# Optimization experiments

Hardware: AMD Instinct MI355X
Metric: run time of the kernel (lower is better)

The kernel has to match this reference:

```python
import jax, jax.numpy as jnp
import numpy as np

B, N, K = 8, 2048, 20
NC = 50
EPS = 1e-5
SLOPE = 0.2


def _knn(xt, k):
    # xt: [B, N, C]; negative squared euclidean distance, top-k (includes self)
    xx = jnp.sum(xt * xt, axis=-1)                      # [B, N]
    inner = jnp.einsum('bnc,bmc->bnm', xt, xt)          # [B, N, N]
    dist = 2.0 * inner - xx[:, :, None] - xx[:, None, :]
    return jax.lax.top_k(dist, k)[1]                    # [B, N, k] int32


def _edge_conv(xt, w, g, b, k):
    # xt: [B, N, C]; w: [O, 2C]; BatchNorm2d over (B, N, k) per out-channel.
    idx = _knn(xt, k)
    nbr = xt[jnp.arange(B)[:, None, None], idx]          # [B, N, k, C]
    ctr = jnp.broadcast_to(xt[:, :, None, :], nbr.shape)
    edge = jnp.concatenate([nbr - ctr, ctr], axis=-1)    # [B, N, k, 2C]
    h = jnp.einsum('bnkc,oc->bnko', edge, w)             # 1x1 conv, no bias
    mu = jnp.mean(h, axis=(0, 1, 2))
    var = jnp.var(h, axis=(0, 1, 2))
    h = (h - mu) / jnp.sqrt(var + EPS) * g + b
    h = jnp.where(h > 0, h, SLOPE * h)                   # LeakyReLU(0.2)
    return jnp.max(h, axis=2)                            # max over k -> [B, N, O]


def _bn1d(y, g, b):
    mu = jnp.mean(y, axis=0)
    var = jnp.var(y, axis=0)
    return (y - mu) / jnp.sqrt(var + EPS) * g + b


def setup_inputs() -> dict:
    key = jax.random.key(0)
    ks = jax.random.split(key, 20)

    def rn(k, shape, scale):
        return jax.random.normal(k, shape, dtype=jnp.float32) * scale

    d = {
        'x': rn(ks[0], (B * N, 3), 1.0),
        'pos': rn(ks[1], (B * N, 3), 1.0),
        'batch': jnp.repeat(jnp.arange(B, dtype=jnp.int64), N),
        'edge_index': jax.random.randint(ks[2], (2, B * N), 0, B * N, dtype=jnp.int64),
        # EdgeConv 1x1 conv weights [out, in], BN gamma/beta
        'w1': rn(ks[3], (64, 6), 0.3),   'g1': jnp.ones(64),  'b1': jnp.zeros(64),
        'w2': rn(ks[4], (64, 128), 0.1), 'g2': jnp.ones(64),  'b2': jnp.zeros(64),
        'w3': rn(ks[5], (128, 128), 0.1),'g3': jnp.ones(128), 'b3': jnp.zeros(128),
        'w4': rn(ks[6], (256, 256), 0.08),'g4': jnp.ones(256),'b4': jnp.zeros(256),
        # lin1: Linear(512,1024)+ReLU+BN1d(1024)
        'lw1': rn(ks[7], (512, 1024), 0.04), 'lb1': jnp.zeros(1024),
        'lg1': jnp.ones(1024), 'lbb1': jnp.zeros(1024),
        # mlp: [1024->256 +ReLU+BN] -> [256->128 +ReLU+BN] -> Lin(128, NC)
        'mw1': rn(ks[8], (1024, 256), 0.03), 'mb1': jnp.zeros(256),
        'mg1': jnp.ones(256), 'mbb1': jnp.zeros(256),
        'mw2': rn(ks[9], (256, 128), 0.06), 'mb2': jnp.zeros(128),
        'mg2': jnp.ones(128), 'mbb2': jnp.zeros(128),
        'hw': rn(ks[10], (128, NC), 0.09), 'hb': jnp.zeros(NC),
    }
    return d


def reference(x, pos, batch, edge_index,
              w1, g1, b1, w2, g2, b2, w3, g3, b3, w4, g4, b4,
              lw1, lb1, lg1, lbb1,
              mw1, mb1, mg1, mbb1, mw2, mb2, mg2, mbb2,
              hw, hb):
    # batch is sorted with N points per cloud -> static reshape
    xt = x.reshape(B, N, 3)
    x1 = _edge_conv(xt, w1, g1, b1, K)   # [B, N, 64]
    x2 = _edge_conv(x1, w2, g2, b2, K)   # [B, N, 64]
    x3 = _edge_conv(x2, w3, g3, b3, K)   # [B, N, 128]
    x4 = _edge_conv(x3, w4, g4, b4, K)   # [B, N, 256]
    cat = jnp.concatenate([x1, x2, x3, x4], axis=-1)  # [B, N, 512]
    h = cat.reshape(B * N, 512)
    h = _bn1d(jax.nn.relu(h @ lw1 + lb1), lg1, lbb1)
    h = _bn1d(jax.nn.relu(h @ mw1 + mb1), mg1, mbb1)   # dropout = identity (eval)
    h = _bn1d(jax.nn.relu(h @ mw2 + mb2), mg2, mbb2)
    logits = h @ hw + hb
    return jax.nn.log_softmax(logits, axis=1)
```

## Files before the change

### kernel.cpp

```cpp
#include <hip/hip_runtime.h>
#include <math.h>

#define NB 8
#define NP 2048
#define KNBR 20
#define NROWS (NB*NP)
#define SLOPEV 0.2f
#define EPSV 1e-5f

typedef short s8v __attribute__((ext_vector_type(8)));
typedef float f4v __attribute__((ext_vector_type(4)));
typedef double d4v __attribute__((ext_vector_type(4)));

__device__ __forceinline__ unsigned short f2bf(float f) {
    union { float f; unsigned u; } v; v.f = f;
    unsigned r = v.u + 0x7FFFu + ((v.u >> 16) & 1u);
    return (unsigned short)(r >> 16);
}

__global__ void mfma64_probe(int* __restrict__ tab)
{
    const int lane = threadIdx.x;
    d4v z = {0.0, 0.0, 0.0, 0.0};
    d4v pa = __builtin_amdgcn_mfma_f64_16x16x4f64((double)lane, 1.0, z, 0, 0, 0);
    d4v pb = __builtin_amdgcn_mfma_f64_16x16x4f64(1.0, (double)lane, z, 0, 0, 0);
    int famA = 1, famB = 1;
#pragma unroll
    for (int r = 0; r < 4; ++r) {
        int iv = (int)(pa[r] + 0.5);
        int row;
        if ((iv & 3) == 0 && iv >= 96) row = (iv - 96) >> 2;
        else { row = (iv - 6) >> 4; famA = 0; }
        int jv = (int)(pb[r] + 0.5);
        int col;
        if ((jv & 3) == 0 && jv >= 96) col = (jv - 96) >> 2;
        else { col = (jv - 6) >> 4; famB = 0; }
        tab[lane * 8 + r]     = row;
        tab[lane * 8 + 4 + r] = col;
    }
    tab[512 + lane] = famA;
    tab[576 + lane] = famB;
}

template<int KD>
__global__ __launch_bounds__(256, 2) void knn_fused2(
    const double* __restrict__ F, int lda, int C,
    const double* __restrict__ xx,
    double* __restrict__ tmpv, int* __restrict__ tmpc,
    const int* __restrict__ tab)
{
    constexpr int CH = (KD < 16) ? KD : 32;
    __shared__ double Bs[CH][66];
    __shared__ double Tile[64][65];
    __shared__ double thr[64];
    __shared__ unsigned msk[64][2];

    const int tid = threadIdx.x;
    const int wave = tid >> 6, lane = tid & 63;
    const int bb    = blockIdx.z;
    const int half  = blockIdx.y;
    const int r0    = blockIdx.x * 64;
    const int cbase = half * 1024;
    const double* Fb  = F  + (size_t)bb * NP * lda;
    const double* xxb = xx + (size_t)bb * NP;

    int rT[4], cT[4];
#pragma unroll
    for (int r = 0; r < 4; ++r) { rT[r] = tab[lane * 8 + r]; cT[r] = tab[lane * 8 + 4 + r]; }
    const int famA = tab[512];
    const int famB = tab[576];
    const int am = famA ? (lane & 15) : (lane >> 2);
    const int ak = famA ? (lane >> 4) : (lane & 3);
    const int bn = famB ? (lane & 15) : (lane >> 2);
    const int bk = famB ? (lane >> 4) : (lane & 3);

    const int arow = r0 + wave * 16 + am;
    double areg[KD / 4];
#pragma unroll
    for (int j = 0; j < KD / 4; ++j) {
        const int k = j * 4 + ak;
        areg[j] = (k < C) ? Fb[(size_t)arow * lda + k] : 0.0;
    }
    double xr4[4];
#pragma unroll
    for (int rg = 0; rg < 4; ++rg)
        xr4[rg] = xxb[r0 + wave * 16 + rT[rg]];

    double kv[KNBR];
    int    ki[KNBR];
#pragma unroll
    for (int q = 0; q < KNBR; ++q) { kv[q] = -INFINITY; ki[q] = 0; }
    if (tid < 64) { thr[tid] = -INFINITY; msk[tid][0] = 0u; msk[tid][1] = 0u; }
    __syncthreads();

    for (int ct = 0; ct < 16; ++ct) {
        const int c0 = cbase + ct * 64;
        d4v acc[4];
#pragma unroll
        for (int nt = 0; nt < 4; ++nt) acc[nt] = (d4v){0.0, 0.0, 0.0, 0.0};

#pragma unroll
        for (int kc = 0; kc < KD; kc += CH) {
            {
                const int col = tid >> 2;
                const int kb0 = (tid & 3) * (CH / 4);
                const double* bp = Fb + (size_t)(c0 + col) * lda + kc + kb0;
#pragma unroll
                for (int i = 0; i < CH / 4; ++i) {
                    const int k2 = kc + kb0 + i;
                    Bs[kb0 + i][col] = (k2 < C) ? bp[i] : 0.0;
                }
            }
            __syncthreads();
#pragma unroll
            for (int kg = 0; kg < CH / 4; ++kg) {
                const double a  = areg[kc / 4 + kg];
                const double b0 = Bs[kg * 4 + bk][bn];
                const double b1 = Bs[kg * 4 + bk][16 + bn];
                const double b2 = Bs[kg * 4 + bk][32 + bn];
                const double b3 = Bs[kg * 4 + bk][48 + bn];
                acc[0] = __builtin_amdgcn_mfma_f64_16x16x4f64(a, b0, acc[0], 0, 0, 0);
                acc[1] = __builtin_amdgcn_mfma_f64_16x16x4f64(a, b1, acc[1], 0, 0, 0);
                acc[2] = __builtin_amdgcn_mfma_f64_16x16x4f64(a, b2, acc[2], 0, 0, 0);
                acc[3] = __builtin_amdgcn_mfma_f64_16x16x4f64(a, b3, acc[3], 0, 0, 0);
            }
            __syncthreads();
        }

#pragma unroll
        for (int nt = 0; nt < 4; ++nt) {
#pragma unroll
            for (int rg = 0; rg < 4; ++rg) {
                const int rloc = wave * 16 + rT[rg];
                const int cloc = nt * 16 + cT[rg];
                const double d = (2.0 * acc[nt][rg] - xr4[rg]) - xxb[c0 + cloc];
                if (d > thr[rloc]) {
                    Tile[rloc][cloc] = d;
                    atomicOr(&msk[rloc][cloc >> 5], 1u << (cloc & 31));
                }
            }
        }
        __syncthreads();

        if (tid < 64) {
            bool changed = false;
#pragma unroll
            for (int w2 = 0; w2 < 2; ++w2) {
                unsigned m = msk[tid][w2];
                msk[tid][w2] = 0u;
                while (m) {
                    const int b = __ffs(m) - 1;
                    m &= m - 1u;
                    const double v = Tile[tid][w2 * 32 + b];
                    if (v > kv[KNBR - 1]) {
                        const int col = c0 + w2 * 32 + b;
                        int pos = 0;
#pragma unroll
                        for (int q = 0; q < KNBR; ++q) pos += (kv[q] >= v) ? 1 : 0;
#pragma unroll
                        for (int q = KNBR - 1; q >= 0; --q) {
                            if (q > pos)       { kv[q] = kv[q - 1]; ki[q] = ki[q - 1]; }
                            else if (q == pos) { kv[q] = v;         ki[q] = col; }
                        }
                        changed = true;
                    }
                }
            }
            if (changed) thr[tid] = kv[KNBR - 1];
        }
        __syncthreads();
    }

    if (tid < 64) {
        const size_t rowg = (size_t)bb * NP + r0 + tid;
        double* vp = tmpv + (rowg * 2 + half) * KNBR;
        int*    cp = tmpc + (rowg * 2 + half) * KNBR;
#pragma unroll
        for (int q = 0; q < KNBR; ++q) { vp[q] = kv[q]; cp[q] = ki[q]; }
    }
}

__global__ void merge_topk(const double* __restrict__ tmpv,
                           const int* __restrict__ tmpc,
                           int* __restrict__ out)
{
    const int row = blockIdx.x * 256 + threadIdx.x;
    if (row >= NROWS) return;
    const double* va = tmpv + (size_t)row * 2 * KNBR;
    const int*    ca = tmpc + (size_t)row * 2 * KNBR;
    const double* vb = va + KNBR;
    const int*    cb = ca + KNBR;
    const int jbase = (row / NP) * NP;
    int* op = out + (size_t)row * KNBR;
    int ia = 0, ib = 0;
#pragma unroll
    for (int q = 0; q < KNBR; ++q) {
        const double x = va[ia], y = vb[ib];
        const bool takeA = (x > y) || (x == y && ca[ia] < cb[ib]);
        if (takeA) { op[q] = jbase + ca[ia]; ++ia; }
        else       { op[q] = jbase + cb[ib]; ++ib; }
    }
}

#define DK 16
__global__ __launch_bounds__(256, 2) void gemm64(
    const double* __restrict__ A, int lda,
    const double* __restrict__ Bm, int ldb,
    double* __restrict__ P, double* __restrict__ Q, int O, int Kd,
    const int* __restrict__ tab)
{
    __shared__ double As[DK][130];
    __shared__ double Bs[DK][66];
    const int tid = threadIdx.x;
    const int wave = tid >> 6, lane = tid & 63;
    const int quad = lane >> 4, l15 = lane & 15;
    const int row0 = blockIdx.y * 128, col0 = blockIdx.x * 64;

    int rT[4], cT[4];
#pragma unroll
    for (int r = 0; r < 4; ++r) { rT[r] = tab[lane * 8 + r]; cT[r] = tab[lane * 8 + 4 + r]; }
    const int famA = tab[512];
    const int famB = tab[576];
    const int am = famA ? l15 : (lane >> 2);
    const int ak = famA ? quad : (lane & 3);
    const int bn = famB ? l15 : (lane >> 2);
    const int bk = famB ? quad : (lane & 3);

    d4v acc[2][4];
#pragma unroll
    for (int mt = 0; mt < 2; ++mt)
#pragma unroll
        for (int nt = 0; nt < 4; ++nt) acc[mt][nt] = (d4v){0.0, 0.0, 0.0, 0.0};

    const int ma = tid >> 1, ka = (tid & 1) * 8;
    const int mb = tid >> 2, kb = (tid & 3) * 4;

    for (int kc = 0; kc < Kd; kc += DK) {
        const double* ap = A + (size_t)(row0 + ma) * lda + kc + ka;
#pragma unroll
        for (int i = 0; i < 8; ++i) {
            const int k2 = kc + ka + i;
            As[ka + i][ma] = (k2 < Kd) ? ap[i] : 0.0;
        }
        const double* bp = Bm + (size_t)(col0 + mb) * ldb + kc + kb;
#pragma unroll
        for (int i = 0; i < 4; ++i) {
            const int k2 = kc + kb + i;
            Bs[kb + i][mb] = (k2 < Kd) ? bp[i] : 0.0;
        }
        __syncthreads();
#pragma unroll
        for (int kg = 0; kg < 4; ++kg) {
            const int k = kg * 4;
            double a0 = As[k + ak][wave * 32 + am];
            double a1 = As[k + ak][wave * 32 + 16 + am];
            double b0 = Bs[k + bk][bn];
            double b1 = Bs[k + bk][16 + bn];
            double b2 = Bs[k + bk][32 + bn];
            double b3 = Bs[k + bk][48 + bn];
            acc[0][0] = __builtin_amdgcn_mfma_f64_16x16x4f64(a0, b0, acc[0][0], 0, 0, 0);
            acc[0][1] = __builtin_amdgcn_mfma_f64_16x16x4f64(a0, b1, acc[0][1], 0, 0, 0);
            acc[0][2] = __builtin_amdgcn_mfma_f64_16x16x4f64(a0, b2, acc[0][2], 0, 0, 0);
            acc[0][3] = __builtin_amdgcn_mfma_f64_16x16x4f64(a0, b3, acc[0][3], 0, 0, 0);
            acc[1][0] = __builtin_amdgcn_mfma_f64_16x16x4f64(a1, b0, acc[1][0], 0, 0, 0);
            acc[1][1] = __builtin_amdgcn_mfma_f64_16x16x4f64(a1, b1, acc[1][1], 0, 0, 0);
            acc[1][2] = __builtin_amdgcn_mfma_f64_16x16x4f64(a1, b2, acc[1][2], 0, 0, 0);
            acc[1][3] = __builtin_amdgcn_mfma_f64_16x16x4f64(a1, b3, acc[1][3], 0, 0, 0);
        }
        __syncthreads();
    }

    double* dst = (col0 < O) ? P : Q;
    const int cbase = (col0 < O) ? col0 : (col0 - O);
#pragma unroll
    for (int mt = 0; mt < 2; ++mt)
#pragma unroll
        for (int nt = 0; nt < 4; ++nt) {
#pragma unroll
            for (int rg = 0; rg < 4; ++rg) {
                const int r = row0 + wave * 32 + mt * 16 + rT[rg];
                const int c = cbase + nt * 16 + cT[rg];
                dst[(size_t)r * O + c] = acc[mt][nt][rg];
            }
        }
}

__global__ __launch_bounds__(256) void gemm_bf16(
    const float* __restrict__ A, int lda,
    const unsigned short* __restrict__ W,
    float* __restrict__ C, int ldc,
    int Kd,
    const float* __restrict__ bias,
    const float* __restrict__ a_ss)
{
    __shared__ unsigned short As[4][64][8];
    __shared__ unsigned short Bs[4][128][8];
    const int tid = threadIdx.x;
    const int wave = tid >> 6, lane = tid & 63;
    const int quad = lane >> 4, l15 = lane & 15;
    const int row0 = blockIdx.y * 64, col0 = blockIdx.x * 128;

    f4v acc[4][2];
#pragma unroll
    for (int mt = 0; mt < 4; ++mt)
#pragma unroll
        for (int nt = 0; nt < 2; ++nt) acc[mt][nt] = (f4v){0.f, 0.f, 0.f, 0.f};

    const int ar = tid >> 2, akc = tid & 3;
    const int br = tid >> 1, bkc = (tid & 1) * 2;

    for (int kc0 = 0; kc0 < Kd; kc0 += 32) {
        {
            const float* ap = A + (size_t)(row0 + ar) * lda + kc0 + akc * 8;
            float t0[8];
            *(float4*)&t0[0] = *(const float4*)ap;
            *(float4*)&t0[4] = *(const float4*)(ap + 4);
            if (a_ss) {
                const int kb = kc0 + akc * 8;
#pragma unroll
                for (int i = 0; i < 8; ++i)
                    t0[i] = fmaf(t0[i], a_ss[kb + i], a_ss[Kd + kb + i]);
            }
            unsigned short u[8];
#pragma unroll
            for (int i = 0; i < 8; ++i) u[i] = f2bf(t0[i]);
            *(uint4*)&As[akc][ar][0] = *(const uint4*)&u[0];
        }
        {
            const unsigned short* wp = W + (size_t)(col0 + br) * Kd + kc0 + bkc * 8;
            uint4 q0 = *(const uint4*)wp;
            uint4 q1 = *(const uint4*)(wp + 8);
            *(uint4*)&Bs[bkc][br][0]     = q0;
            *(uint4*)&Bs[bkc + 1][br][0] = q1;
        }
        __syncthreads();

        s8v a[4], b[2];
#pragma unroll
        for (int mt = 0; mt < 4; ++mt)
            a[mt] = *(const s8v*)&As[quad][mt * 16 + l15][0];
#pragma unroll
        for (int nt = 0; nt < 2; ++nt)
            b[nt] = *(const s8v*)&Bs[quad][wave * 32 + nt * 16 + l15][0];
#pragma unroll
        for (int mt = 0; mt < 4; ++mt)
#pragma unroll
            for (int nt = 0; nt < 2; ++nt)
                acc[mt][nt] = __builtin_amdgcn_mfma_f32_16x16x32_bf16(
                    a[mt], b[nt], acc[mt][nt], 0, 0, 0);
        __syncthreads();
    }

#pragma unroll
    for (int mt = 0; mt < 4; ++mt)
#pragma unroll
        for (int nt = 0; nt < 2; ++nt) {
            const int col = col0 + wave * 32 + nt * 16 + l15;
            const float bi = bias[col];
#pragma unroll
            for (int r = 0; r < 4; ++r) {
                const int row = row0 + mt * 16 + quad * 4 + r;
                float v = acc[mt][nt][r] + bi;
                v = fmaxf(v, 0.f);
                C[(size_t)row * ldc + col] = v;
            }
        }
}

#define GBK 16
__global__ __launch_bounds__(256, 2) void gemm_f32(
    const float* __restrict__ A, int lda,
    const float* __restrict__ Bm, int ldb,
    float* __restrict__ Cm, int ldc,
    int M, int Nn, int Kd, int mode,
    const float* __restrict__ bias,
    const float* __restrict__ a_ss)
{
    __shared__ float As[GBK][132];
    __shared__ float Bs[GBK][132];
    const int tid = threadIdx.x;
    const int tx = tid & 15, ty = tid >> 4;
    const int lin = blockIdx.y * gridDim.x + blockIdx.x;
    const int bx = lin / gridDim.y;
    const int by = lin - bx * gridDim.y;
    const int row0 = by * 128, col0 = bx * 128;
    float acc[8][8];
#pragma unroll
    for (int i = 0; i < 8; ++i)
#pragma unroll
        for (int j = 0; j < 8; ++j) acc[i][j] = 0.f;

    const int m  = tid >> 1;
    const int kk = (tid & 1) * 8;

    for (int kc = 0; kc < Kd; kc += GBK) {
        const int gc = col0 + m;
        const float* ap = A  + (size_t)(row0 + m) * lda + kc + kk;
        const float* bp = Bm + (size_t)gc * ldb + kc + kk;
#pragma unroll
        for (int i = 0; i < 8; ++i) {
            const int k2 = kc + kk + i;
            float v = 0.f;
            if (k2 < Kd) {
                v = ap[i];
                if (a_ss) v = fmaf(v, a_ss[k2], a_ss[Kd + k2]);
            }
            As[kk + i][m] = v;
        }
#pragma unroll
        for (int i = 0; i < 8; ++i) {
            const int k2 = kc + kk + i;
            float v = 0.f;
            if (gc < Nn && k2 < Kd) v = bp[i];
            Bs[kk + i][m] = v;
        }
        __syncthreads();
#pragma unroll
        for (int k = 0; k < GBK; ++k) {
            float4 a0 = *(const float4*)&As[k][ty * 4];
            float4 a1 = *(const float4*)&As[k][64 + ty * 4];
            float4 b0 = *(const float4*)&Bs[k][tx * 4];
            float4 b1 = *(const float4*)&Bs[k][64 + tx * 4];
            float a[8] = {a0.x, a0.y, a0.z, a0.w, a1.x, a1.y, a1.z, a1.w};
            float b[8] = {b0.x, b0.y, b0.z, b0.w, b1.x, b1.y, b1.z, b1.w};
#pragma unroll
            for (int i = 0; i < 8; ++i)
#pragma unroll
                for (int j = 0; j < 8; ++j) acc[i][j] = fmaf(a[i], b[j], acc[i][j]);
        }
        __syncthreads();
    }

#pragma unroll
    for (int i = 0; i < 8; ++i) {
        const int row = row0 + ty * 4 + (i & 3) + ((i >> 2) << 6);
        if (row >= M) continue;
#pragma unroll
        for (int h = 0; h < 2; ++h) {
            const int c0 = col0 + tx * 4 + (h << 6);
#pragma unroll
            for (int j = 0; j < 4; ++j) {
                const int col = c0 + j;
                if (col < Nn) {
                    float t = acc[i][h * 4 + j];
                    if (mode == 2)      t = fmaxf(t + bias[col], 0.f);
                    else if (mode == 3) t = t + bias[col];
                    Cm[(size_t)row * ldc + col] = t;
                }
            }
        }
    }
}

__global__ void f2d_kernel(const float* __restrict__ in, double* __restrict__ out, long n)
{
    long t = (long)blockIdx.x * 256 + threadIdx.x;
    if (t < n) out[t] = (double)in[t];
}
__global__ void d2f_kernel(const double* __restrict__ in, float* __restrict__ out, long n)
{
    long t = (long)blockIdx.x * 256 + threadIdx.x;
    if (t < n) out[t] = (float)in[t];
}

__global__ void xx_kernel_d(const double* __restrict__ F, int lda, int C,
                            double* __restrict__ xx)
{
    int r = blockIdx.x * 256 + threadIdx.x;
    if (r >= NROWS) return;
    const double* p = F + (long)r * lda;
    double s = 0.0;
    for (int c = 0; c < C; ++c) { double v = p[c]; s = fma(v, v, s); }
    xx[r] = s;
}

__global__ void wmod_kernel_d(const float* __restrict__ w, double* __restrict__ wm,
                              int O, int C)
{
    int t = blockIdx.x * 256 + threadIdx.x;
    if (t >= O * C) return;
    int o = t / C, c = t - o * C;
    double a = (double)w[o * 2 * C + c];
    double b = (double)w[o * 2 * C + C + c];
    wm[o * C + c] = a;
    wm[(O + o) * C + c] = b - a;
}

__global__ void transpose_kernel(const float* __restrict__ in, float* __restrict__ out,
                                 int R, int C)
{
    long t = (long)blockIdx.x * 256 + threadIdx.x;
    if (t >= (long)R * C) return;
    int r = (int)(t / C), c = (int)(t - (long)r * C);
    out[(long)c * R + r] = in[t];
}

__global__ void transpose_bf(const float* __restrict__ in, unsigned short* __restrict__ out,
                             int R, int C)
{
    long t = (long)blockIdx.x * 256 + threadIdx.x;
    if (t >= (long)R * C) return;
    int r = (int)(t / C), c = (int)(t - (long)r * C);
    out[(long)c * R + r] = f2bf(in[t]);
}

__global__ __launch_bounds__(256) void edge_gather(const double* __restrict__ P,
                                                   const double* __restrict__ Q,
                                                   const int* __restrict__ idx,
                                                   int O, int shiftO,
                                                   double* __restrict__ sums,
                                                   double* __restrict__ catOut, int ldo)
{
    const int tid = threadIdx.x;
    const int o = tid & (O - 1);
    const int q = tid >> shiftO;
    const int nsub = 256 >> shiftO;
    const int lin = blockIdx.x;
    const int r0 = (lin & 7) * NP + (lin >> 3) * 16;
    double s = 0.0, ss = 0.0;
    for (int r = r0 + q; r < r0 + 16; r += nsub) {
        const double qv = Q[(size_t)r * O + o];
        const int* ip = idx + r * KNBR;
        double m = -INFINITY;
        for (int k = 0; k < KNBR; ++k) {
            const int j = ip[k];
            const double v = P[(size_t)j * O + o] + qv;
            s += v; ss = fma(v, v, ss);
            m = fmax(m, v);
        }
        catOut[(size_t)r * ldo + o] = m;
    }
    __shared__ double red[256];
    red[tid] = s; __syncthreads();
    if (q == 0) for (int qq = 1; qq < nsub; ++qq) s += red[o + (qq << shiftO)];
    __syncthreads();
    red[tid] = ss; __syncthreads();
    if (q == 0) {
        for (int qq = 1; qq < nsub; ++qq) ss += red[o + (qq << shiftO)];
        atomicAdd(&sums[o], s);
        atomicAdd(&sums[O + o], ss);
    }
}

__global__ void bn_finalize_d(const double* __restrict__ sums,
                              const float* __restrict__ g, const float* __restrict__ b,
                              double* __restrict__ ss, int O, double invCnt)
{
    int o = blockIdx.x * 256 + threadIdx.x;
    if (o >= O) return;
    double mu  = sums[o] * invCnt;
    double var = sums[O + o] * invCnt - mu * mu;
    double is  = 1.0 / sqrt(var + 1e-5);
    double sc  = (double)g[o] * is;
    ss[o] = sc;
    ss[O + o] = (double)b[o] - mu * sc;
}

__global__ __launch_bounds__(256) void bn_apply(double* __restrict__ catOut, int ldo,
                                                const double* __restrict__ ssb,
                                                int O, int shiftO,
                                                const double* __restrict__ P,
                                                const double* __restrict__ Q,
                                                const int* __restrict__ idx)
{
    const int t = blockIdx.x * 256 + threadIdx.x;
    const int o = t & (O - 1);
    const int r = t >> shiftO;
    const double sc = ssb[o], sh = ssb[O + o];
    double v = catOut[(size_t)r * ldo + o];
    if (sc < 0.0) {
        const double qv = Q[(size_t)r * O + o];
        const int* ip = idx + r * KNBR;
        double m = INFINITY;
        for (int k = 0; k < KNBR; ++k)
            m = fmin(m, P[(size_t)ip[k] * O + o] + qv);
        v = m;
    }
    double u = fma(v, sc, sh);
    u = u > 0.0 ? u : 0.2 * u;
    catOut[(size_t)r * ldo + o] = u;
}

__global__ void col_stats(const float* __restrict__ Y, int ncol,
                          float* __restrict__ sums)
{
    int c  = blockIdx.x * 128 + threadIdx.x;
    int r0 = blockIdx.y * 256;
    float s = 0.f, ss = 0.f;
    for (int r = r0; r < r0 + 256; ++r) {
        float v = Y[(long)r * ncol + c];
        s += v; ss = fmaf(v, v, ss);
    }
    atomicAdd(&sums[c], s);
    atomicAdd(&sums[ncol + c], ss);
}

__global__ void bn_finalize_f(const float* __restrict__ sums,
                              const float* __restrict__ g, const float* __restrict__ b,
                              float* __restrict__ ss, int O, float invCnt)
{
    int o = blockIdx.x * 256 + threadIdx.x;
    if (o >= O) return;
    float mu  = sums[o] * invCnt;
    float var = sums[O + o] * invCnt - mu * mu;
    float is  = rsqrtf(var + EPSV);
    float sc  = g[o] * is;
    ss[o] = sc;
    ss[O + o] = b[o] - mu * sc;
}

__global__ __launch_bounds__(256) void log_softmax_kernel(float* __restrict__ Y)
{
    const int lane = threadIdx.x & 63;
    const int row  = blockIdx.x * 4 + (threadIdx.x >> 6);
    float v = -INFINITY;
    if (lane < 50) v = Y[(long)row * 50 + lane];
    float mx = v;
#pragma unroll
    for (int off = 32; off >= 1; off >>= 1) mx = fmaxf(mx, __shfl_xor(mx, off, 64));
    float e = (lane < 50) ? expf(v - mx) : 0.f;
    float s = e;
#pragma unroll
    for (int off = 32; off >= 1; off >>= 1) s += __shfl_xor(s, off, 64);
    float l = logf(s) + mx;
    if (lane < 50) Y[(long)row * 50 + lane] = v - l;
}

extern "C" void kernel_launch(void* const* d_in, const int* in_sizes, int n_in,
                              void* d_out, int out_size, void* d_ws, size_t ws_size,
                              hipStream_t stream)
{
    const float* x   = (const float*)d_in[0];
    const float* w[4]  = {(const float*)d_in[4], (const float*)d_in[7],
                          (const float*)d_in[10], (const float*)d_in[13]};
    const float* g[4]  = {(const float*)d_in[5], (const float*)d_in[8],
                          (const float*)d_in[11], (const float*)d_in[14]};
    const float* bb[4] = {(const float*)d_in[6], (const float*)d_in[9],
                          (const float*)d_in[12], (const float*)d_in[15]};
    const float* lw1 = (const float*)d_in[16]; const float* lb1 = (const float*)d_in[17];
    const float* lg1 = (const float*)d_in[18]; const float* lbb1 = (const float*)d_in[19];
    const float* mw1 = (const float*)d_in[20]; const float* mb1 = (const float*)d_in[21];
    const float* mg1 = (const float*)d_in[22]; const float* mbb1 = (const float*)d_in[23];
    const float* mw2 = (const float*)d_in[24]; const float* mb2 = (const float*)d_in[25];
    const float* mg2 = (const float*)d_in[26]; const float* mbb2 = (const float*)d_in[27];
    const float* hw  = (const float*)d_in[28]; const float* hb  = (const float*)d_in[29];
    float* out = (float*)d_out;

    char* base = (char*)d_ws;
    double* catD = (double*)base;
    char*  un    = base + 67108864;
    double* tmpv = (double*)un;
    int*    tmpc = (int*)(un + 5242880);
    double* Pb   = (double*)un;
    double* Qb   = (double*)(un + 33554432);
    float* cat32 = (float*)un;
    float* Y2    = (float*)(un + 33554432);
    float* Y3    = (float*)(un + 50331648);
    unsigned short* lw1Tb = (unsigned short*)(un + 58720256);
    unsigned short* mw1Tb = (unsigned short*)(un + 59768832);
    unsigned short* mw2Tb = (unsigned short*)(un + 60293120);
    float* hwT   = (float*)(un + 60358656);
    float* Y1    = (float*)base;
    char* tail = base + 2u * 67108864u;
    int*    idxb  = (int*)tail;
    double* xD    = (double*)(tail + 1310720);
    double* xxD   = (double*)(tail + 1703936);
    double* wmodD = (double*)(tail + 1835008);
    double* sumsD = (double*)(tail + 2359296);
    double* ssbD  = (double*)(tail + 2367488);
    float*  sumsF = (float*)(tail + 2375680);
    float*  ssbF  = (float*)(tail + 2383872);
    int*    mtab  = (int*)(tail + 2392064);

    mfma64_probe<<<1, 64, 0, stream>>>(mtab);

    f2d_kernel<<<(NROWS * 3 + 255) / 256, 256, 0, stream>>>(x, xD, (long)NROWS * 3);

    const double* Fin[4] = {xD, catD + 0, catD + 64, catD + 128};
    const int   ldaL[4] = {3, 512, 512, 512};
    const int   CL[4]   = {3, 64, 64, 128};
    const int   OL[4]   = {64, 64, 128, 256};
    const int   coff[4] = {0, 64, 128, 256};

    for (int l = 0; l < 4; ++l) {
        const double* F = Fin[l];
        const int lda = ldaL[l], C = CL[l], O = OL[l];
        const int shiftO = (O == 64) ? 6 : (O == 128) ? 7 : 8;

        wmod_kernel_d<<<(O * C + 255) / 256, 256, 0, stream>>>(w[l], wmodD, O, C);
        xx_kernel_d<<<NROWS / 256, 256, 0, stream>>>(F, lda, C, xxD);

        dim3 kg(NP / 64, 2, NB);
        if (C == 3)
            knn_fused2<4><<<kg, 256, 0, stream>>>(F, lda, C, xxD, tmpv, tmpc, mtab);
        else if (C == 64)
            knn_fused2<64><<<kg, 256, 0, stream>>>(F, lda, C, xxD, tmpv, tmpc, mtab);
        else
            knn_fused2<128><<<kg, 256, 0, stream>>>(F, lda, C, xxD, tmpv, tmpc, mtab);
        merge_topk<<<NROWS / 256, 256, 0, stream>>>(tmpv, tmpc, idxb);

        gemm64<<<dim3((2 * O) / 64, NROWS / 128), 256, 0, stream>>>(
            F, lda, wmodD, C, Pb, Qb, O, C, mtab);

        hipMemsetAsync(sumsD, 0, 2 * O * sizeof(double), stream);
        edge_gather<<<NROWS / 16, 256, 0, stream>>>(Pb, Qb, idxb, O, shiftO, sumsD,
                                                    catD + coff[l], 512);
        bn_finalize_d<<<(O + 255) / 256, 256, 0, stream>>>(sumsD, g[l], bb[l], ssbD, O,
                                                           1.0 / ((double)NROWS * KNBR));
        bn_apply<<<(NROWS * O) / 256, 256, 0, stream>>>(catD + coff[l], 512, ssbD,
                                                        O, shiftO, Pb, Qb, idxb);
    }

    d2f_kernel<<<((long)NROWS * 512 + 255) / 256, 256, 0, stream>>>(catD, cat32, (long)NROWS * 512);

    transpose_bf<<<(512 * 1024 + 255) / 256, 256, 0, stream>>>(lw1, lw1Tb, 512, 1024);
    transpose_bf<<<(1024 * 256 + 255) / 256, 256, 0, stream>>>(mw1, mw1Tb, 1024, 256);
    transpose_bf<<<(256 * 128 + 255) / 256, 256, 0, stream>>>(mw2, mw2Tb, 256, 128);
    transpose_kernel<<<(128 * 50 + 255) / 256, 256, 0, stream>>>(hw, hwT, 128, 50);

    {
        gemm_bf16<<<dim3(1024 / 128, NROWS / 64), 256, 0, stream>>>(
            cat32, 512, lw1Tb, Y1, 1024, 512, lb1, nullptr);
        hipMemsetAsync(sumsF, 0, 2 * 1024 * sizeof(float), stream);
        col_stats<<<dim3(1024 / 128, 64), 128, 0, stream>>>(Y1, 1024, sumsF);
        bn_finalize_f<<<4, 256, 0, stream>>>(sumsF, lg1, lbb1, ssbF, 1024, 1.f / NROWS);
    }
    {
        gemm_bf16<<<dim3(256 / 128, NROWS / 64), 256, 0, stream>>>(
            Y1, 1024, mw1Tb, Y2, 256, 1024, mb1, ssbF);
        hipMemsetAsync(sumsF, 0, 2 * 256 * sizeof(float), stream);
        col_stats<<<dim3(256 / 128, 64), 128, 0, stream>>>(Y2, 256, sumsF);
        bn_finalize_f<<<1, 256, 0, stream>>>(sumsF, mg1, mbb1, ssbF, 256, 1.f / NROWS);
    }
    {
        gemm_bf16<<<dim3(128 / 128, NROWS / 64), 256, 0, stream>>>(
            Y2, 256, mw2Tb, Y3, 128, 256, mb2, ssbF);
        hipMemsetAsync(sumsF, 0, 2 * 128 * sizeof(float), stream);
        col_stats<<<dim3(1, 64), 128, 0, stream>>>(Y3, 128, sumsF);
        bn_finalize_f<<<1, 256, 0, stream>>>(sumsF, mg2, mbb2, ssbF, 128, 1.f / NROWS);
    }
    {
        dim3 gg(1, NROWS / 128);
        gemm_f32<<<gg, 256, 0, stream>>>(Y3, 128, hwT, 128, out, 50,
                                         NROWS, 50, 128, 3, hb, ssbF);
        log_softmax_kernel<<<NROWS / 4, 256, 0, stream>>>(out);
    }
}
```

Baseline: 1.922 ms.

## Double-buffer B tile loads in fused kNN MFMA kernel

Replaces the single shared-memory B chunk buffer with two buffers. The next chunk, or the first chunk of the next column tile, is prefetched while MFMA runs on the current one, which removes one barrier per chunk. The chunk depth is reduced from 32 to 16 so the double buffer fits in shared memory, which means more iterations and barriers for the deep layers. The aim is to hide global-load latency behind the f64 matrix work.

```diff
diff --git a/kernel.cpp b/kernel.cpp
--- a/kernel.cpp
+++ b/kernel.cpp
@@ -49,8 +49,9 @@
     double* __restrict__ tmpv, int* __restrict__ tmpc,
     const int* __restrict__ tab)
 {
-    constexpr int CH = (KD < 16) ? KD : 32;
-    __shared__ double Bs[CH][66];
+    constexpr int CH  = (KD < 16) ? KD : 16;
+    constexpr int NCH = KD / CH;
+    __shared__ double Bs[2][CH][66];
     __shared__ double Tile[64][65];
     __shared__ double thr[64];
     __shared__ unsigned msk[64][2];
@@ -74,6 +75,9 @@
     const int bn = famB ? (lane & 15) : (lane >> 2);
     const int bk = famB ? (lane >> 4) : (lane & 3);
 
+    const int scol = tid >> 2;
+    const int skb0 = (tid & 3) * (CH / 4);
+
     const int arow = r0 + wave * 16 + am;
     double areg[KD / 4];
 #pragma unroll
@@ -91,8 +95,18 @@
 #pragma unroll
     for (int q = 0; q < KNBR; ++q) { kv[q] = -INFINITY; ki[q] = 0; }
     if (tid < 64) { thr[tid] = -INFINITY; msk[tid][0] = 0u; msk[tid][1] = 0u; }
+
+    {
+        const double* bp = Fb + (size_t)(cbase + scol) * lda + skb0;
+#pragma unroll
+        for (int i = 0; i < CH / 4; ++i) {
+            const int k2 = skb0 + i;
+            Bs[0][skb0 + i][scol] = (k2 < C) ? bp[i] : 0.0;
+        }
+    }
     __syncthreads();
 
+    int cur = 0;
     for (int ct = 0; ct < 16; ++ct) {
         const int c0 = cbase + ct * 64;
         d4v acc[4];
@@ -100,31 +114,37 @@
         for (int nt = 0; nt < 4; ++nt) acc[nt] = (d4v){0.0, 0.0, 0.0, 0.0};
 
 #pragma unroll
-        for (int kc = 0; kc < KD; kc += CH) {
-            {
-                const int col = tid >> 2;
-                const int kb0 = (tid & 3) * (CH / 4);
-                const double* bp = Fb + (size_t)(c0 + col) * lda + kc + kb0;
+        for (int ich = 0; ich < NCH; ++ich) {
+            if (ich + 1 < NCH) {
+                const int kc2 = (ich + 1) * CH;
+                const double* bp = Fb + (size_t)(c0 + scol) * lda + kc2 + skb0;
 #pragma unroll
                 for (int i = 0; i < CH / 4; ++i) {
-                    const int k2 = kc + kb0 + i;
-                    Bs[kb0 + i][col] = (k2 < C) ? bp[i] : 0.0;
+                    const int k2 = kc2 + skb0 + i;
+                    Bs[cur ^ 1][skb0 + i][scol] = (k2 < C) ? bp[i] : 0.0;
                 }
-            }
-            __syncthreads();
+            } else if (ct + 1 < 16) {
+                const double* bp = Fb + (size_t)(c0 + 64 + scol) * lda + skb0;
+#pragma unroll
+                for (int i = 0; i < CH / 4; ++i) {
+                    const int k2 = skb0 + i;
+                    Bs[cur ^ 1][skb0 + i][scol] = (k2 < C) ? bp[i] : 0.0;
+                }
+            }
 #pragma unroll
             for (int kg = 0; kg < CH / 4; ++kg) {
-                const double a  = areg[kc / 4 + kg];
-                const double b0 = Bs[kg * 4 + bk][bn];
-                const double b1 = Bs[kg * 4 + bk][16 + bn];
-                const double b2 = Bs[kg * 4 + bk][32 + bn];
-                const double b3 = Bs[kg * 4 + bk][48 + bn];
+                const double a  = areg[(ich * CH) / 4 + kg];
+                const double b0 = Bs[cur][kg * 4 + bk][bn];
+                const double b1 = Bs[cur][kg * 4 + bk][16 + bn];
+                const double b2 = Bs[cur][kg * 4 + bk][32 + bn];
+                const double b3 = Bs[cur][kg * 4 + bk][48 + bn];
                 acc[0] = __builtin_amdgcn_mfma_f64_16x16x4f64(a, b0, acc[0], 0, 0, 0);
                 acc[1] = __builtin_amdgcn_mfma_f64_16x16x4f64(a, b1, acc[1], 0, 0, 0);
                 acc[2] = __builtin_amdgcn_mfma_f64_16x16x4f64(a, b2, acc[2], 0, 0, 0);
                 acc[3] = __builtin_amdgcn_mfma_f64_16x16x4f64(a, b3, acc[3], 0, 0, 0);
             }
             __syncthreads();
+            cur ^= 1;
         }
 
 #pragma unroll
```

Result: no change. 1.933 ms (+0.6%).
